# Kernel tuning notes

Measured on AMD Instinct MI355X. Metric: run time of the kernel, lower is better.

The kernel has to match this reference:

```python
import jax, jax.numpy as jnp
import numpy as np

D_MODEL = 512
N_HEADS = 8
HEAD_DIM = D_MODEL // N_HEADS
NEG_INF = -1e9


def setup_inputs() -> dict:
    key = jax.random.key(0)
    ks = jax.random.split(key, 12)
    B, N, M = 8, 2048, 2048
    inp = {
        'query': jax.random.normal(ks[0], (B, D_MODEL, N), jnp.float32),
        'key': jax.random.normal(ks[1], (B, D_MODEL, M), jnp.float32),
        'value': jax.random.normal(ks[2], (B, D_MODEL, M), jnp.float32),
        'query_mask': jnp.ones((B, N), jnp.float32),
        'key_value_mask': jnp.ones((B, M), jnp.float32),
        # Conv1d(d_model, d_model, kernel_size=1) == pointwise linear: W [out, in], b [out]
        'Wq': jax.random.normal(ks[3], (D_MODEL, D_MODEL), jnp.float32) / np.sqrt(D_MODEL),
        'bq': jax.random.normal(ks[4], (D_MODEL,), jnp.float32) * 0.01,
        'Wk': jax.random.normal(ks[5], (D_MODEL, D_MODEL), jnp.float32) / np.sqrt(D_MODEL),
        'bk': jax.random.normal(ks[6], (D_MODEL,), jnp.float32) * 0.01,
        'Wv': jax.random.normal(ks[7], (D_MODEL, D_MODEL), jnp.float32) / np.sqrt(D_MODEL),
        'bv': jax.random.normal(ks[8], (D_MODEL,), jnp.float32) * 0.01,
        'Wm': jax.random.normal(ks[9], (D_MODEL, D_MODEL), jnp.float32) / np.sqrt(D_MODEL),
        'bm': jax.random.normal(ks[10], (D_MODEL,), jnp.float32) * 0.01,
    }
    return inp


def _pointwise(W, b, x):
    # Conv1d k=1 over [B, C_in, N] -> [B, C_out, N]
    return jnp.einsum('oi,bin->bon', W, x) + b[None, :, None]


def reference(query, key, value, query_mask, key_value_mask,
              Wq, bq, Wk, bk, Wv, bv, Wm, bm):
    B = query.shape[0]
    N = query.shape[2]
    M = key.shape[2]
    # project and split heads: [B, head_dim, n_heads, seq]
    q = _pointwise(Wq, bq, query).reshape(B, HEAD_DIM, N_HEADS, N)
    k = _pointwise(Wk, bk, key).reshape(B, HEAD_DIM, N_HEADS, M)
    v = _pointwise(Wv, bv, value).reshape(B, HEAD_DIM, N_HEADS, M)
    # scores [B, H, N, M], scaled by sqrt(head_dim) (query.shape[1] post-split)
    scores = jnp.einsum('bdhn,bdhm->bhnm', q, k) / jnp.sqrt(jnp.float32(HEAD_DIM))
    # dual mask: outer product of key_value_mask [B,1,1,M] and query_mask [B,1,N,1]
    mask = key_value_mask[:, None, None, :] * query_mask[:, None, :, None]
    scores = jnp.where(mask > 0, scores, NEG_INF)
    prob = jax.nn.softmax(scores, axis=-1)  # [B, H, N, M]
    x = jnp.einsum('bhnm,bdhm->bdhn', prob, v)  # [B, head_dim, H, N]
    out = _pointwise(Wm, bm, x.reshape(B, D_MODEL, N))
    return out
```

## Files before the change

kernel.cpp:

```cpp
#include <hip/hip_runtime.h>


typedef _Float16 f16;
typedef _Float16 f16x4 __attribute__((ext_vector_type(4)));
typedef _Float16 f16x8 __attribute__((ext_vector_type(8)));
typedef float f32x4 __attribute__((ext_vector_type(4)));

#define D_MODEL 512
#define HD 64
#define SEQ 2048
#define QSCL 0.18033688011112042f
#define KVNEG -1.4426950409e9f
#define FMAXB -6.0f

__global__ __launch_bounds__(256) void k_transpose(
    const float* __restrict__ q, const float* __restrict__ k, const float* __restrict__ v,
    f16* __restrict__ XT)
{
  __shared__ __align__(16) f16 Ts[64][72];
  int t = threadIdx.x;
  int nt = blockIdx.x, ct = blockIdx.y, z = blockIdx.z;
  int src = z >> 3, b = z & 7;
  const float* S = (src == 0) ? q : (src == 1) ? k : v;
  {
    int cr = t >> 2, ns = t & 3;
    const float* p = S + ((size_t)b * D_MODEL + ct * 64 + cr) * SEQ + nt * 64 + ns * 16;
    f32x4 a0 = *(const f32x4*)(p);
    f32x4 a1 = *(const f32x4*)(p + 4);
    f32x4 a2 = *(const f32x4*)(p + 8);
    f32x4 a3 = *(const f32x4*)(p + 12);
    f16x8 h0, h1;
#pragma unroll
    for (int j = 0; j < 4; ++j) { h0[j] = (f16)a0[j]; h0[4 + j] = (f16)a1[j]; h1[j] = (f16)a2[j]; h1[4 + j] = (f16)a3[j]; }
    *(f16x8*)&Ts[cr][ns * 16] = h0;
    *(f16x8*)&Ts[cr][ns * 16 + 8] = h1;
  }
  __syncthreads();
  {
    int nr = t >> 2, cs = t & 3;
    f16x8 h0, h1;
#pragma unroll
    for (int j = 0; j < 8; ++j) h0[j] = Ts[cs * 16 + j][nr];
#pragma unroll
    for (int j = 0; j < 8; ++j) h1[j] = Ts[cs * 16 + 8 + j][nr];
    f16* dst = XT + (((size_t)z) * SEQ + nt * 64 + nr) * D_MODEL + ct * 64 + cs * 16;
    *(f16x8*)dst = h0;
    *(f16x8*)(dst + 8) = h1;
  }
}

__global__ __launch_bounds__(256) void k_wconv(
    const float* __restrict__ Wq, const float* __restrict__ Wk, const float* __restrict__ Wv,
    const float* __restrict__ Wm, const float* __restrict__ kvmask,
    f16* __restrict__ W3, f16* __restrict__ Wmh, float* __restrict__ biasArr)
{
  int idx = blockIdx.x * 256 + threadIdx.x;
  if (idx < 262144) {
    W3[idx] = (f16)Wq[idx];
    W3[262144 + idx] = (f16)Wk[idx];
    W3[524288 + idx] = (f16)Wv[idx];
    int o = idx >> 9, c = idx & 511;
    int h = c & 7, d = c >> 3;
    Wmh[((size_t)h * 512 + o) * 64 + d] = (f16)Wm[idx];
  }
  if (idx < 16384) {
    biasArr[idx] = (kvmask[idx] > 0.f) ? FMAXB : KVNEG;
  }
}

__global__ __launch_bounds__(256, 2) void k_proj(
    const f16* __restrict__ W3, const float* __restrict__ bq, const float* __restrict__ bk,
    const float* __restrict__ bv, const f16* __restrict__ XT,
    f16* __restrict__ Qt, f16* __restrict__ Kt, f16* __restrict__ Vh)
{
  __shared__ __align__(16) char smem[36864];
  f16 (*As)[72] = (f16(*)[72])smem;
  f16 (*Bs)[72] = (f16(*)[72])(smem + 18432);
  f16 (*Ls)[136] = (f16(*)[136])smem;

  int t = threadIdx.x;
  int proj = blockIdx.z, b = blockIdx.y;
  int ot = blockIdx.x & 3, ntile = blockIdx.x >> 2;
  int w = t >> 6, ln = t & 63, i16 = ln & 15, q4 = ln >> 4;
  int ow = w >> 1, nw = w & 1;

  const f16* Wp = W3 + (size_t)proj * 262144;
  const f16* Xp = XT + ((size_t)proj * 8 + b) * (size_t)SEQ * D_MODEL;

  f32x4 acc[4][4];
#pragma unroll
  for (int x = 0; x < 4; ++x)
#pragma unroll
    for (int y = 0; y < 4; ++y) acc[x][y] = (f32x4){0.f, 0.f, 0.f, 0.f};

  int srow = t >> 1, shalf = t & 1;
  for (int kc = 0; kc < 8; ++kc) {
    __syncthreads();
    const f16* Ap = Wp + ((size_t)(ot * 128 + srow)) * 512 + kc * 64 + shalf * 32;
#pragma unroll
    for (int s8 = 0; s8 < 4; ++s8)
      *(f32x4*)&As[srow][shalf * 32 + s8 * 8] = *(const f32x4*)(Ap + s8 * 8);
    const f16* Bp = Xp + ((size_t)(ntile * 128 + srow)) * 512 + kc * 64 + shalf * 32;
#pragma unroll
    for (int s8 = 0; s8 < 4; ++s8)
      *(f32x4*)&Bs[srow][shalf * 32 + s8 * 8] = *(const f32x4*)(Bp + s8 * 8);
    __syncthreads();
#pragma unroll
    for (int kk = 0; kk < 2; ++kk) {
      f16x8 af[4], bf[4];
#pragma unroll
      for (int x = 0; x < 4; ++x) af[x] = *(const f16x8*)&As[ow * 64 + x * 16 + i16][kk * 32 + q4 * 8];
#pragma unroll
      for (int y = 0; y < 4; ++y) bf[y] = *(const f16x8*)&Bs[nw * 64 + y * 16 + i16][kk * 32 + q4 * 8];
#pragma unroll
      for (int x = 0; x < 4; ++x)
#pragma unroll
        for (int y = 0; y < 4; ++y)
          acc[x][y] = __builtin_amdgcn_mfma_f32_16x16x32_f16(af[x], bf[y], acc[x][y], 0, 0, 0);
    }
  }

  const float* bias = (proj == 0) ? bq : (proj == 1) ? bk : bv;
  float scl = (proj == 0) ? QSCL : 1.0f;
  __syncthreads();
#pragma unroll
  for (int x = 0; x < 4; ++x) {
    f32x4 bb = *(const f32x4*)(bias + ot * 128 + ow * 64 + x * 16 + q4 * 4);
#pragma unroll
    for (int y = 0; y < 4; ++y)
#pragma unroll
      for (int r = 0; r < 4; ++r)
        Ls[ow * 64 + x * 16 + q4 * 4 + r][nw * 64 + y * 16 + i16] = (f16)((acc[x][y][r] + bb[r]) * scl);
  }
  __syncthreads();
  if (proj < 2) {
    f16* dst = (proj == 0) ? Qt : Kt;
    int n = t >> 1, seg = t & 1;
#pragma unroll
    for (int h = 0; h < 8; ++h) {
      f16x8 g;
#pragma unroll
      for (int j = 0; j < 8; ++j) g[j] = Ls[8 * (seg * 8 + j) + h][n];
      f16* dp = dst + (((size_t)((b * 8 + h) * 4 + ot)) * 2048 + ntile * 128 + n) * 16 + seg * 8;
      *(f16x8*)dp = g;
    }
  } else {
#pragma unroll
    for (int p = 0; p < 8; ++p) {
      int ol = (t >> 4) + 16 * p;
      int ch = t & 15;
      int og = ot * 128 + ol;
      int h = og & 7, d = og >> 3;
      f16* dp = Vh + (((size_t)(b * 8 + h)) * HD + d) * SEQ + ntile * 128 + ch * 8;
      *(f32x4*)dp = *(const f32x4*)&Ls[ol][ch * 8];
    }
  }
}

#define ATTN_BODY(IT, Kc, Vc, Kn, Vn)                                                   \
  do {                                                                                  \
    int it_ = (IT);                                                                     \
    if (it_ < 31) {                                                                     \
      *(f32x4*)&Kn[rk0][cx0 * 8] = kA;                                                  \
      *(f32x4*)&Kn[rk1][cx1 * 8] = kB;                                                  \
      *(f32x4*)&Vn[vw0][vc0 * 8] = vA;                                                  \
      *(f32x4*)&Vn[vw1][vc1 * 8] = vB;                                                  \
    }                                                                                   \
    if (it_ < 30) {                                                                     \
      int mo_ = (it_ + 2) * 64;                                                         \
      kA = *(const f32x4*)(ksp0 + (size_t)mo_ * 16);                                    \
      kB = *(const f32x4*)(ksp1 + (size_t)mo_ * 16);                                    \
      vA = *(const f32x4*)(vsp0 + mo_);                                                 \
      vB = *(const f32x4*)(vsp1 + mo_);                                                 \
    }                                                                                   \
    int m0_ = it_ * 64;                                                                 \
    f16x8 pf[2][2];                                                                     \
    float rs0_ = 0.f, rs1_ = 0.f;                                                       \
    _Pragma("unroll")                                                                   \
    for (int p = 0; p < 2; ++p) {                                                       \
      f32x4 bias0 = *(const f32x4*)(bap + m0_ + p * 32 + q4 * 8);                       \
      f32x4 bias1 = *(const f32x4*)(bap + m0_ + p * 32 + 4 + q4 * 8);                   \
      f16x8 kf00 = *(const f16x8*)&Kc[(2 * p) * 16 + i16][q4 * 8];                      \
      f16x8 kf01 = *(const f16x8*)&Kc[(2 * p) * 16 + i16][32 + q4 * 8];                 \
      f16x8 kf10 = *(const f16x8*)&Kc[(2 * p + 1) * 16 + i16][q4 * 8];                  \
      f16x8 kf11 = *(const f16x8*)&Kc[(2 * p + 1) * 16 + i16][32 + q4 * 8];             \
      __builtin_amdgcn_s_setprio(1);                                                    \
      f32x4 s00 = __builtin_amdgcn_mfma_f32_16x16x32_f16(kf00, qf[0][0], bias0, 0, 0, 0); \
      s00 = __builtin_amdgcn_mfma_f32_16x16x32_f16(kf01, qf[0][1], s00, 0, 0, 0);       \
      f32x4 s01 = __builtin_amdgcn_mfma_f32_16x16x32_f16(kf10, qf[0][0], bias1, 0, 0, 0); \
      s01 = __builtin_amdgcn_mfma_f32_16x16x32_f16(kf11, qf[0][1], s01, 0, 0, 0);       \
      f32x4 s10 = __builtin_amdgcn_mfma_f32_16x16x32_f16(kf00, qf[1][0], bias0, 0, 0, 0); \
      s10 = __builtin_amdgcn_mfma_f32_16x16x32_f16(kf01, qf[1][1], s10, 0, 0, 0);       \
      f32x4 s11 = __builtin_amdgcn_mfma_f32_16x16x32_f16(kf10, qf[1][0], bias1, 0, 0, 0); \
      s11 = __builtin_amdgcn_mfma_f32_16x16x32_f16(kf11, qf[1][1], s11, 0, 0, 0);       \
      __builtin_amdgcn_s_setprio(0);                                                    \
      f16x8 pv0, pv1;                                                                   \
      _Pragma("unroll")                                                                 \
      for (int r = 0; r < 4; ++r) {                                                     \
        float e00 = __builtin_amdgcn_exp2f(s00[r]);                                     \
        float e01 = __builtin_amdgcn_exp2f(s01[r]);                                     \
        float e10 = __builtin_amdgcn_exp2f(s10[r]);                                     \
        float e11 = __builtin_amdgcn_exp2f(s11[r]);                                     \
        rs0_ += e00 + e01;                                                              \
        rs1_ += e10 + e11;                                                              \
        pv0[r] = (f16)e00; pv0[4 + r] = (f16)e01;                                       \
        pv1[r] = (f16)e10; pv1[4 + r] = (f16)e11;                                       \
      }                                                                                 \
      pf[p][0] = pv0;                                                                   \
      pf[p][1] = pv1;                                                                   \
    }                                                                                   \
    rsum2[0] += rs0_;                                                                   \
    rsum2[1] += rs1_;                                                                   \
    __builtin_amdgcn_s_setprio(1);                                                      \
    _Pragma("unroll")                                                                   \
    for (int dt = 0; dt < 4; ++dt) {                                                    \
      f16x8 vf0 = *(const f16x8*)&Vc[dt * 16 + i16][q4 * 8];                            \
      f16x8 vf1 = *(const f16x8*)&Vc[dt * 16 + i16][32 + q4 * 8];                       \
      _Pragma("unroll")                                                                 \
      for (int nt = 0; nt < 2; ++nt) {                                                  \
        f32x4 o = acc_o[dt][nt];                                                        \
        o = __builtin_amdgcn_mfma_f32_16x16x32_f16(vf0, pf[0][nt], o, 0, 0, 0);         \
        o = __builtin_amdgcn_mfma_f32_16x16x32_f16(vf1, pf[1][nt], o, 0, 0, 0);         \
        acc_o[dt][nt] = o;                                                              \
      }                                                                                 \
    }                                                                                   \
    __builtin_amdgcn_s_setprio(0);                                                      \
    __syncthreads();                                                                    \
  } while (0)

__global__ __launch_bounds__(256, 2) void k_attn(
    const f16* __restrict__ Qt, const f16* __restrict__ Kt, const f16* __restrict__ Vh,
    const float* __restrict__ qmask, const float* __restrict__ biasArr,
    f16* __restrict__ O)
{
  __shared__ __align__(16) char smem[36864];
  f16 (*Qs)[72] = (f16(*)[72])smem;
  f16 (*Ks0)[72] = (f16(*)[72])(smem);
  f16 (*Vs0)[72] = (f16(*)[72])(smem + 9216);
  f16 (*Ks1)[72] = (f16(*)[72])(smem + 18432);
  f16 (*Vs1)[72] = (f16(*)[72])(smem + 27648);

  int t = threadIdx.x;
  int bh = blockIdx.x >> 4;
  int b = bh >> 3;
  int n0 = (blockIdx.x & 15) * 128;
  int w = t >> 6, ln = t & 63, i16 = ln & 15, q4 = ln >> 4;

  const f16* Qb = Qt + (size_t)bh * 131072;
  const f16* Kb = Kt + (size_t)bh * 131072;
  const f16* Vb = Vh + (size_t)bh * HD * SEQ;
  const float* bap = biasArr + (size_t)b * SEQ;

  int tid0 = t, tid1 = 256 + t;
  int cx0 = tid0 >> 6, nk0 = tid0 & 63;
  int cx1 = tid1 >> 6, nk1 = tid1 & 63;
  int rk0 = (nk0 & 32) | ((nk0 & 4) << 2) | ((nk0 >> 1) & 12) | (nk0 & 3);
  int rk1 = (nk1 & 32) | ((nk1 & 4) << 2) | ((nk1 >> 1) & 12) | (nk1 & 3);
  int vw0 = tid0 >> 3, vc0 = tid0 & 7;
  int vw1 = tid1 >> 3, vc1 = tid1 & 7;
  const f16* ksp0 = Kb + ((size_t)((cx0 >> 1) * 2048 + nk0)) * 16 + (cx0 & 1) * 8;
  const f16* ksp1 = Kb + ((size_t)((cx1 >> 1) * 2048 + nk1)) * 16 + (cx1 & 1) * 8;
  const f16* vsp0 = Vb + (size_t)vw0 * SEQ + vc0 * 8;
  const f16* vsp1 = Vb + (size_t)vw1 * SEQ + vc1 * 8;

  f32x4 kA = *(const f32x4*)(ksp0);
  f32x4 kB = *(const f32x4*)(ksp1);
  f32x4 vA = *(const f32x4*)(vsp0);
  f32x4 vB = *(const f32x4*)(vsp1);

#pragma unroll
  for (int p = 0; p < 4; ++p) {
    int tid = p * 256 + t;
    int n = tid & 127, cx = tid >> 7;
    *(f32x4*)&Qs[n][cx * 8] =
        *(const f32x4*)(Qb + ((size_t)((cx >> 1) * 2048 + n0 + n)) * 16 + (cx & 1) * 8);
  }
  __syncthreads();
  f16x8 qf[2][2];
#pragma unroll
  for (int nt = 0; nt < 2; ++nt)
#pragma unroll
    for (int kc = 0; kc < 2; ++kc)
      qf[nt][kc] = *(const f16x8*)&Qs[w * 32 + nt * 16 + i16][kc * 32 + q4 * 8];
#pragma unroll
  for (int nt = 0; nt < 2; ++nt) {
    float qok = qmask[(size_t)b * SEQ + n0 + w * 32 + nt * 16 + i16];
    f16 qz = (qok > 0.f) ? (f16)1 : (f16)0;
    qf[nt][0] *= qz;
    qf[nt][1] *= qz;
  }
  __syncthreads();

  *(f32x4*)&Ks0[rk0][cx0 * 8] = kA;
  *(f32x4*)&Ks0[rk1][cx1 * 8] = kB;
  *(f32x4*)&Vs0[vw0][vc0 * 8] = vA;
  *(f32x4*)&Vs0[vw1][vc1 * 8] = vB;
  kA = *(const f32x4*)(ksp0 + (size_t)64 * 16);
  kB = *(const f32x4*)(ksp1 + (size_t)64 * 16);
  vA = *(const f32x4*)(vsp0 + 64);
  vB = *(const f32x4*)(vsp1 + 64);
  __syncthreads();

  f32x4 acc_o[4][2];
#pragma unroll
  for (int dt = 0; dt < 4; ++dt)
#pragma unroll
    for (int nt = 0; nt < 2; ++nt) acc_o[dt][nt] = (f32x4){0.f, 0.f, 0.f, 0.f};
  float rsum2[2] = {0.f, 0.f};

  for (int ot = 0; ot < 16; ++ot) {
    ATTN_BODY(2 * ot, Ks0, Vs0, Ks1, Vs1);
    ATTN_BODY(2 * ot + 1, Ks1, Vs1, Ks0, Vs0);
  }

  f16 (*Os)[72] = (f16(*)[72])(smem + w * 4608);
#pragma unroll
  for (int nt = 0; nt < 2; ++nt) {
    float l = rsum2[nt];
    l += __shfl_xor(l, 16, 64);
    l += __shfl_xor(l, 32, 64);
    float inv = 1.f / l;
#pragma unroll
    for (int dt = 0; dt < 4; ++dt) {
      f16x4 o4;
#pragma unroll
      for (int r = 0; r < 4; ++r) o4[r] = (f16)(acc_o[dt][nt][r] * inv);
      *(f16x4*)&Os[nt * 16 + i16][dt * 16 + q4 * 4] = o4;
    }
  }
  __syncthreads();
  f16* Ob = O + ((size_t)bh * SEQ + n0 + w * 32) * HD;
#pragma unroll
  for (int p = 0; p < 4; ++p) {
    int row = (ln >> 3) + 8 * p, ch = ln & 7;
    *(f32x4*)(Ob + (size_t)row * HD + ch * 8) = *(const f32x4*)&Os[row][ch * 8];
  }
}

__global__ __launch_bounds__(256, 2) void k_out(
    const f16* __restrict__ Wmh, const float* __restrict__ bm,
    const f16* __restrict__ O, float* __restrict__ out)
{
  __shared__ __align__(16) char smem[20480];
  f16 (*As)[40] = (f16(*)[40])smem;
  f16 (*Bs)[40] = (f16(*)[40])(smem + 10240);

  int t = threadIdx.x;
  int b = blockIdx.y;
  int ot = blockIdx.x & 3, ntile = blockIdx.x >> 2;
  int w = t >> 6, ln = t & 63, i16 = ln & 15, q4 = ln >> 4;
  int ow = w >> 1, nw = w & 1;

  f32x4 acc[4][4];
#pragma unroll
  for (int x = 0; x < 4; ++x)
#pragma unroll
    for (int y = 0; y < 4; ++y) acc[x][y] = (f32x4){0.f, 0.f, 0.f, 0.f};

  int srow = t >> 1, sseg = t & 1;
  for (int ck = 0; ck < 16; ++ck) {
    int h = ck >> 1, dc = ck & 1;
    __syncthreads();
    const f16* Ap = Wmh + ((size_t)h * 512 + ot * 128 + srow) * 64 + dc * 32 + sseg * 16;
    *(f32x4*)&As[srow][sseg * 16] = *(const f32x4*)(Ap);
    *(f32x4*)&As[srow][sseg * 16 + 8] = *(const f32x4*)(Ap + 8);
    const f16* Bp = O + (((size_t)(b * 8 + h)) * SEQ + ntile * 128 + srow) * 64 + dc * 32 + sseg * 16;
    *(f32x4*)&Bs[srow][sseg * 16] = *(const f32x4*)(Bp);
    *(f32x4*)&Bs[srow][sseg * 16 + 8] = *(const f32x4*)(Bp + 8);
    __syncthreads();
    f16x8 af[4], bf[4];
#pragma unroll
    for (int x = 0; x < 4; ++x) af[x] = *(const f16x8*)&As[ow * 64 + x * 16 + i16][q4 * 8];
#pragma unroll
    for (int y = 0; y < 4; ++y) bf[y] = *(const f16x8*)&Bs[nw * 64 + y * 16 + i16][q4 * 8];
#pragma unroll
    for (int x = 0; x < 4; ++x)
#pragma unroll
      for (int y = 0; y < 4; ++y)
        acc[x][y] = __builtin_amdgcn_mfma_f32_16x16x32_f16(af[x], bf[y], acc[x][y], 0, 0, 0);
  }

#pragma unroll
  for (int x = 0; x < 4; ++x) {
    f32x4 bb = *(const f32x4*)(bm + ot * 128 + ow * 64 + x * 16 + q4 * 4);
#pragma unroll
    for (int y = 0; y < 4; ++y)
#pragma unroll
      for (int r = 0; r < 4; ++r) {
        int o_g = ot * 128 + ow * 64 + x * 16 + q4 * 4 + r;
        int n_g = ntile * 128 + nw * 64 + y * 16 + i16;
        out[((size_t)b * 512 + o_g) * SEQ + n_g] = acc[x][y][r] + bb[r];
      }
  }
}

extern "C" void kernel_launch(void* const* d_in, const int* in_sizes, int n_in,
                              void* d_out, int out_size, void* d_ws, size_t ws_size,
                              hipStream_t stream)
{
  const float* query  = (const float*)d_in[0];
  const float* key    = (const float*)d_in[1];
  const float* value  = (const float*)d_in[2];
  const float* qmask  = (const float*)d_in[3];
  const float* kvmask = (const float*)d_in[4];
  const float* Wq = (const float*)d_in[5];
  const float* bq = (const float*)d_in[6];
  const float* Wk = (const float*)d_in[7];
  const float* bk = (const float*)d_in[8];
  const float* Wv = (const float*)d_in[9];
  const float* bv = (const float*)d_in[10];
  const float* Wm = (const float*)d_in[11];
  const float* bm = (const float*)d_in[12];
  float* out = (float*)d_out;

  char* ws = (char*)d_ws;
  f16* XT  = (f16*)(ws);
  f16* Qt  = (f16*)(ws + 50331648);
  f16* Kt  = (f16*)(ws + 67108864);
  f16* Vh  = (f16*)(ws + 83886080);
  f16* Oat = (f16*)(ws);
  f16* W3  = (f16*)(ws + 100663296);
  f16* Wmh = (f16*)(ws + 102236160);
  float* biasArr = out;

  k_transpose<<<dim3(32, 8, 24), 256, 0, stream>>>(query, key, value, XT);
  k_wconv<<<1024, 256, 0, stream>>>(Wq, Wk, Wv, Wm, kvmask, W3, Wmh, biasArr);
  k_proj<<<dim3(64, 8, 3), 256, 0, stream>>>(W3, bq, bk, bv, XT, Qt, Kt, Vh);
  k_attn<<<1024, 256, 0, stream>>>(Qt, Kt, Vh, qmask, biasArr, Oat);
  k_out<<<dim3(64, 8), 256, 0, stream>>>(Wmh, bm, Oat, out);
}
```

Measured before the change: 316.0 us.

## Stage K/V tiles via direct global-to-LDS loads with XOR-swizzled layout

Replaces the register-staged K/V prefetch (global load into registers, then ds_write one iteration later) with global_load_lds direct-to-LDS copies issued one tile ahead. It drops the padded 72-column LDS rows for unpadded 64-column rows with an XOR swizzle to avoid bank conflicts, and remaps block IDs so blocks sharing a batch-head are spread differently. This frees the VGPRs and ds_write work of the old staging path. The risk is that the wait on the direct loads at the barrier (vmcnt) may expose global-load latency, since only one tile of lookahead remains.

Result: faster. 309.7 us (-2.0%).

```diff
diff --git a/kernel.cpp b/kernel.cpp
--- a/kernel.cpp
+++ b/kernel.cpp
@@ -12,6 +12,12 @@
 #define QSCL 0.18033688011112042f
 #define KVNEG -1.4426950409e9f
 #define FMAXB -6.0f
+
+__device__ __forceinline__ void gload16(const f16* g, f16* l) {
+  __builtin_amdgcn_global_load_lds(
+      (const __attribute__((address_space(1))) void*)g,
+      (__attribute__((address_space(3))) void*)l, 16, 0, 0);
+}
 
 __global__ __launch_bounds__(256) void k_transpose(
     const float* __restrict__ q, const float* __restrict__ k, const float* __restrict__ v,
@@ -157,22 +163,20 @@
   }
 }
 
+#define STAGE_TILE(Kn, Vn, IT)                                   \
+  do {                                                           \
+    size_t ok_ = (size_t)(IT) * 1024;                            \
+    size_t ov_ = (size_t)(IT) * 64;                              \
+    gload16(kS0 + ok_, &Kn[w * 16][0]);                          \
+    gload16(kS1 + ok_, &Kn[w * 16 + 8][0]);                      \
+    gload16(vS0 + ov_, &Vn[w * 16][0]);                          \
+    gload16(vS1 + ov_, &Vn[w * 16 + 8][0]);                      \
+  } while (0)
+
 #define ATTN_BODY(IT, Kc, Vc, Kn, Vn)                                                   \
   do {                                                                                  \
     int it_ = (IT);                                                                     \
-    if (it_ < 31) {                                                                     \
-      *(f32x4*)&Kn[rk0][cx0 * 8] = kA;                                                  \
-      *(f32x4*)&Kn[rk1][cx1 * 8] = kB;                                                  \
-      *(f32x4*)&Vn[vw0][vc0 * 8] = vA;                                                  \
-      *(f32x4*)&Vn[vw1][vc1 * 8] = vB;                                                  \
-    }                                                                                   \
-    if (it_ < 30) {                                                                     \
-      int mo_ = (it_ + 2) * 64;                                                         \
-      kA = *(const f32x4*)(ksp0 + (size_t)mo_ * 16);                                    \
-      kB = *(const f32x4*)(ksp1 + (size_t)mo_ * 16);                                    \
-      vA = *(const f32x4*)(vsp0 + mo_);                                                 \
-      vB = *(const f32x4*)(vsp1 + mo_);                                                 \
-    }                                                                                   \
+    if (it_ < 31) STAGE_TILE(Kn, Vn, it_ + 1);                                          \
     int m0_ = it_ * 64;                                                                 \
     f16x8 pf[2][2];                                                                     \
     float rs0_ = 0.f, rs1_ = 0.f;                                                       \
@@ -180,14 +184,14 @@
     for (int p = 0; p < 2; ++p) {                                                       \
       f32x4 bias0 = *(const f32x4*)(bap + m0_ + p * 32 + q4 * 8);                       \
       f32x4 bias1 = *(const f32x4*)(bap + m0_ + p * 32 + 4 + q4 * 8);                   \
-      f16x8 kf00 = *(const f16x8*)&Kc[(2 * p) * 16 + i16][q4 * 8];                      \
-      f16x8 kf01 = *(const f16x8*)&Kc[(2 * p) * 16 + i16][32 + q4 * 8];                 \
-      f16x8 kf10 = *(const f16x8*)&Kc[(2 * p + 1) * 16 + i16][q4 * 8];                  \
-      f16x8 kf11 = *(const f16x8*)&Kc[(2 * p + 1) * 16 + i16][32 + q4 * 8];             \
+      f16x8 kf00 = *(const f16x8*)&Kc[(2 * p) * 16 + i16][c0];                          \
+      f16x8 kf01 = *(const f16x8*)&Kc[(2 * p) * 16 + i16][c1];                          \
+      f16x8 kf10 = *(const f16x8*)&Kc[(2 * p + 1) * 16 + i16][c0];                      \
+      f16x8 kf11 = *(const f16x8*)&Kc[(2 * p + 1) * 16 + i16][c1];                      \
       __builtin_amdgcn_s_setprio(1);                                                    \
       f32x4 s00 = __builtin_amdgcn_mfma_f32_16x16x32_f16(kf00, qf[0][0], bias0, 0, 0, 0); \
       s00 = __builtin_amdgcn_mfma_f32_16x16x32_f16(kf01, qf[0][1], s00, 0, 0, 0);       \
-      f32x4 s01 = __builtin_amdgcn_mfma_f32_16x16x32_f16(kf10, qf[0][0], bias1, 0, 0, 0); \
+      f32x4 s01 = __builtin_amdgcn_mfma_f32_16x16x32_f16(kf10, qf[1 - 1][0], bias1, 0, 0, 0); \
       s01 = __builtin_amdgcn_mfma_f32_16x16x32_f16(kf11, qf[0][1], s01, 0, 0, 0);       \
       f32x4 s10 = __builtin_amdgcn_mfma_f32_16x16x32_f16(kf00, qf[1][0], bias0, 0, 0, 0); \
       s10 = __builtin_amdgcn_mfma_f32_16x16x32_f16(kf01, qf[1][1], s10, 0, 0, 0);       \
@@ -214,8 +218,8 @@
     __builtin_amdgcn_s_setprio(1);                                                      \
     _Pragma("unroll")                                                                   \
     for (int dt = 0; dt < 4; ++dt) {                                                    \
-      f16x8 vf0 = *(const f16x8*)&Vc[dt * 16 + i16][q4 * 8];                            \
-      f16x8 vf1 = *(const f16x8*)&Vc[dt * 16 + i16][32 + q4 * 8];                       \
+      f16x8 vf0 = *(const f16x8*)&Vc[dt * 16 + i16][c0];                                \
+      f16x8 vf1 = *(const f16x8*)&Vc[dt * 16 + i16][c1];                                \
       _Pragma("unroll")                                                                 \
       for (int nt = 0; nt < 2; ++nt) {                                                  \
         f32x4 o = acc_o[dt][nt];                                                        \
@@ -233,17 +237,19 @@
     const float* __restrict__ qmask, const float* __restrict__ biasArr,
     f16* __restrict__ O)
 {
-  __shared__ __align__(16) char smem[36864];
+  __shared__ __align__(16) char smem[32768];
   f16 (*Qs)[72] = (f16(*)[72])smem;
-  f16 (*Ks0)[72] = (f16(*)[72])(smem);
-  f16 (*Vs0)[72] = (f16(*)[72])(smem + 9216);
-  f16 (*Ks1)[72] = (f16(*)[72])(smem + 18432);
-  f16 (*Vs1)[72] = (f16(*)[72])(smem + 27648);
+  f16 (*Ks0)[64] = (f16(*)[64])(smem);
+  f16 (*Vs0)[64] = (f16(*)[64])(smem + 8192);
+  f16 (*Ks1)[64] = (f16(*)[64])(smem + 16384);
+  f16 (*Vs1)[64] = (f16(*)[64])(smem + 24576);
 
   int t = threadIdx.x;
-  int bh = blockIdx.x >> 4;
+  int bid = blockIdx.x;
+  int slot = bid >> 3;
+  int bh = (bid & 7) * 8 + (slot >> 4);
   int b = bh >> 3;
-  int n0 = (blockIdx.x & 15) * 128;
+  int n0 = (slot & 15) * 128;
   int w = t >> 6, ln = t & 63, i16 = ln & 15, q4 = ln >> 4;
 
   const f16* Qb = Qt + (size_t)bh * 131072;
@@ -251,22 +257,21 @@
   const f16* Vb = Vh + (size_t)bh * HD * SEQ;
   const float* bap = biasArr + (size_t)b * SEQ;
 
-  int tid0 = t, tid1 = 256 + t;
-  int cx0 = tid0 >> 6, nk0 = tid0 & 63;
-  int cx1 = tid1 >> 6, nk1 = tid1 & 63;
-  int rk0 = (nk0 & 32) | ((nk0 & 4) << 2) | ((nk0 >> 1) & 12) | (nk0 & 3);
-  int rk1 = (nk1 & 32) | ((nk1 & 4) << 2) | ((nk1 >> 1) & 12) | (nk1 & 3);
-  int vw0 = tid0 >> 3, vc0 = tid0 & 7;
-  int vw1 = tid1 >> 3, vc1 = tid1 & 7;
-  const f16* ksp0 = Kb + ((size_t)((cx0 >> 1) * 2048 + nk0)) * 16 + (cx0 & 1) * 8;
-  const f16* ksp1 = Kb + ((size_t)((cx1 >> 1) * 2048 + nk1)) * 16 + (cx1 & 1) * 8;
-  const f16* vsp0 = Vb + (size_t)vw0 * SEQ + vc0 * 8;
-  const f16* vsp1 = Vb + (size_t)vw1 * SEQ + vc1 * 8;
-
-  f32x4 kA = *(const f32x4*)(ksp0);
-  f32x4 kB = *(const f32x4*)(ksp1);
-  f32x4 vA = *(const f32x4*)(vsp0);
-  f32x4 vB = *(const f32x4*)(vsp1);
+  const f16 *kS0, *kS1, *vS0, *vS1;
+  {
+    int p = ln & 7;
+    int r0 = w * 16 + (ln >> 3);
+    int r1 = r0 + 8;
+    int cK0 = p ^ (r0 & 7), cK1 = p ^ (r1 & 7);
+    int m0k = (r0 & 35) | ((r0 & 16) >> 2) | ((r0 & 8) << 1) | ((r0 & 4) << 1);
+    int m1k = (r1 & 35) | ((r1 & 16) >> 2) | ((r1 & 8) << 1) | ((r1 & 4) << 1);
+    kS0 = Kb + ((size_t)((cK0 >> 1) * 2048 + m0k)) * 16 + (cK0 & 1) * 8;
+    kS1 = Kb + ((size_t)((cK1 >> 1) * 2048 + m1k)) * 16 + (cK1 & 1) * 8;
+    vS0 = Vb + (size_t)r0 * SEQ + cK0 * 8;
+    vS1 = Vb + (size_t)r1 * SEQ + cK1 * 8;
+  }
+  int c0 = ((q4) ^ (i16 & 7)) * 8;
+  int c1 = ((q4 + 4) ^ (i16 & 7)) * 8;
 
 #pragma unroll
   for (int p = 0; p < 4; ++p) {
@@ -291,14 +296,7 @@
   }
   __syncthreads();
 
-  *(f32x4*)&Ks0[rk0][cx0 * 8] = kA;
-  *(f32x4*)&Ks0[rk1][cx1 * 8] = kB;
-  *(f32x4*)&Vs0[vw0][vc0 * 8] = vA;
-  *(f32x4*)&Vs0[vw1][vc1 * 8] = vB;
-  kA = *(const f32x4*)(ksp0 + (size_t)64 * 16);
-  kB = *(const f32x4*)(ksp1 + (size_t)64 * 16);
-  vA = *(const f32x4*)(vsp0 + 64);
-  vB = *(const f32x4*)(vsp1 + 64);
+  STAGE_TILE(Ks0, Vs0, 0);
   __syncthreads();
 
   f32x4 acc_o[4][2];
```
